# Kernel optimization log

Measured on AMD Instinct MI355X. Metric: run time of the kernel, lower is better.

Reference implementation:

```python
import jax, jax.numpy as jnp
import numpy as np

L = 16            # num_levels
F = 2             # features per level
T = 1 << 19       # hashmap size
BASE = 16         # base resolution
RES = 512         # desired_resolution (outer trilinear grid)
N_PTS = 262144

# 8 corner offsets of a unit cube, [8,3]
OFFS = np.array([[(c >> 0) & 1, (c >> 1) & 1, (c >> 2) & 1] for c in range(8)], dtype=np.uint32)
OFFS_J = jnp.asarray(OFFS)
OFFS_B = jnp.asarray(OFFS.astype(bool))
P1 = jnp.uint32(2654435761)
P2 = jnp.uint32(805459861)


def hash_encode(x01, table):
    """Instant-NGP multiresolution hash encoding. x01: [N,3] in [0,1]. table: [L,T,F]."""
    feats = []
    for l in range(L):
        res = BASE * (2 ** l)
        pos = x01 * res                      # [N,3]
        p0 = jnp.floor(pos)
        frac = pos - p0                      # [N,3]
        corners = p0.astype(jnp.uint32)[:, None, :] + OFFS_J[None]   # [N,8,3]
        if (res + 1) ** 3 <= T:              # dense level
            c = jnp.minimum(corners, jnp.uint32(res))
            idx = c[..., 0] + c[..., 1] * jnp.uint32(res + 1) + c[..., 2] * jnp.uint32((res + 1) * (res + 1))
        else:                                # hashed level (spatial hash, xor of primes)
            idx = corners[..., 0] ^ (corners[..., 1] * P1) ^ (corners[..., 2] * P2)
            idx = idx & jnp.uint32(T - 1)
        g = table[l][idx.astype(jnp.int32)]  # [N,8,F]
        w = jnp.where(OFFS_B[None], frac[:, None, :], 1.0 - frac[:, None, :]).prod(-1)  # [N,8]
        feats.append(jnp.einsum('nc,ncf->nf', w, g))
    return jnp.concatenate(feats, axis=-1)   # [N, L*F]


def mlp(x, W0, W1, W2):
    h = jax.nn.relu(x @ W0)
    h = jax.nn.relu(h @ W1)
    return h @ W2


def setup_inputs() -> dict:
    key = jax.random.key(0)
    k1, k2, k3, k4, k5 = jax.random.split(key, 5)
    xyz = jax.random.uniform(k1, (N_PTS, 3), dtype=jnp.float32, minval=-1.0, maxval=1.0)
    table = jax.random.uniform(k2, (L, T, F), dtype=jnp.float32, minval=-1e-4, maxval=1e-4)
    W0 = jax.random.normal(k3, (L * F, 64), dtype=jnp.float32) * (1.0 / np.sqrt(L * F))
    W1 = jax.random.normal(k4, (64, 64), dtype=jnp.float32) * (1.0 / 8.0)
    W2 = jax.random.normal(k5, (64, 8), dtype=jnp.float32) * (1.0 / 8.0)
    return {"xyz": xyz, "table": table, "W0": W0, "W1": W1, "W2": W2, "bound": 1}


def reference(xyz, table, W0, W1, W2, bound):
    xn = (xyz + bound) / (2 * bound)          # [N,3] in [0,1]
    coords = xn * RES
    c0 = jnp.clip(jnp.floor(coords), 0.0, RES - 1.0)   # [N,3] floats holding ints
    frac = coords - c0                         # u,v,w per-axis [N,3]
    out = jnp.zeros((xyz.shape[0], 8), dtype=xyz.dtype)
    for b in range(8):
        bits = np.array([(b >> 0) & 1, (b >> 1) & 1, (b >> 2) & 1], dtype=np.float32)
        cc = (c0 + bits) / RES                 # corner point normalized to [0,1]
        f = mlp(hash_encode(cc, table), W0, W1, W2)   # [N,8]
        w = jnp.where(bits.astype(bool), frac, 1.0 - frac).prod(-1)  # [N]
        out = out + w[:, None] * f
    return out
```

## Files before the change

### kernel.cpp

```cpp
#include <hip/hip_runtime.h>


typedef __attribute__((ext_vector_type(8))) short short8_t;
typedef __attribute__((ext_vector_type(4))) float f32x4;

static constexpr unsigned kT    = 1u << 19;
static constexpr unsigned kMask = kT - 1u;
static constexpr unsigned cP1   = 2654435761u;
static constexpr unsigned cP2   = 805459861u;
static constexpr int      BLOCK = 256;
static constexpr int      WOFF  = 4096;
static constexpr int      TOFF  = 4096;
static constexpr size_t   WS_NEED = ((size_t)TOFF + (1u << 21)) * 4;

static __device__ __forceinline__ unsigned bf16_rn(float x) {
    unsigned u = __float_as_uint(x);
    return (u + 0x7fffu + ((u >> 16) & 1u)) >> 16;
}

static __device__ __forceinline__ float2 bf2dec(unsigned u) {
    return make_float2(__uint_as_float(u << 16),
                       __uint_as_float(u & 0xffff0000u));
}

static __device__ __forceinline__ f32x4 mfma16(short8_t a, short8_t b, f32x4 c) {
    return __builtin_amdgcn_mfma_f32_16x16x32_bf16(a, b, c, 0, 0, 0);
}

__global__ void prep_w(const float* __restrict__ W0, const float* __restrict__ W1,
                       const float* __restrict__ W2, uint4* __restrict__ ws)
{
    const int t = blockIdx.x, lane = threadIdx.x;
    const int n = lane & 15, q = lane >> 4;
    unsigned hi[4];
    #pragma unroll
    for (int d = 0; d < 4; ++d) {
        unsigned h2[2];
        #pragma unroll
        for (int s = 0; s < 2; ++s) {
            const int j = d * 2 + s;
            float v;
            if (t < 4) {
                v = W0[(q * 8 + j) * 64 + t * 16 + n];
            } else {
                const int kp = (j < 4) ? (q * 4 + j) : (16 + q * 4 + (j - 4));
                if (t < 12) v = W1[(((t - 4) & 1) * 32 + kp) * 64 + ((t - 4) >> 1) * 16 + n];
                else        v = (n < 8) ? W2[((t - 12) * 32 + kp) * 8 + n] : 0.0f;
            }
            h2[s] = bf16_rn(v);
        }
        hi[d] = h2[0] | (h2[1] << 16);
    }
    ws[t * 64 + lane] = make_uint4(hi[0], hi[1], hi[2], hi[3]);
}

__global__ void conv_c(const float4* __restrict__ src, uint2* __restrict__ dst)
{
    const int i = blockIdx.x * 256 + threadIdx.x;
    const float4 v = src[i];
    dst[i] = make_uint2(bf16_rn(v.x) | (bf16_rn(v.y) << 16),
                        bf16_rn(v.z) | (bf16_rn(v.w) << 16));
}

__global__ void conv_f(const float2* __restrict__ src, unsigned* __restrict__ dst)
{
    const int i = blockIdx.x * 256 + threadIdx.x;
    const unsigned v = (1u << 20) - 1u - (unsigned)i;
    const int s = __clz((int)v) - 12;
    const unsigned fo = (1u << 20) - ((1u << 20) >> s);
    const unsigned j = (unsigned)i - fo;
    const float2 e = src[((size_t)(5 + s) << 19) + ((size_t)j << s)];
    dst[i] = bf16_rn(e.x) | (bf16_rn(e.y) << 16);
}

template<bool BT>
__global__ __launch_bounds__(BLOCK, 5)
void ngp_mfma(const float*  __restrict__ xyz,
              const float2* __restrict__ tbl,
              const int*    __restrict__ boundp,
              const unsigned* __restrict__ wsw,
              float*        __restrict__ out,
              int npts)
{
    __shared__ __align__(16) unsigned lds[7680];
    const int tid  = threadIdx.x;
    const int lane = tid & 63;
    const int wv   = tid >> 6;

    {
        const uint4* __restrict__ wsrc = (const uint4*)wsw;
        uint4* wdst = (uint4*)(lds + WOFF);
        #pragma unroll
        for (int k = 0; k < 4; ++k) {
            const int i = tid + k * 256;
            if (i < 896) wdst[i] = wsrc[i];
        }
    }

    const unsigned* __restrict__ tbx = wsw + TOFF;

    const int ge = blockIdx.x * BLOCK + tid;
    const int pt = ge >> 3;
    const int b  = ge & 7;

    const float bnd = (float)boundp[0];
    const float sc  = 0.5f / bnd;

    const float pxv = xyz[pt * 3 + 0];
    const float pyv = xyz[pt * 3 + 1];
    const float pzv = xyz[pt * 3 + 2];

    const float cxf = (pxv + bnd) * sc * 512.0f;
    const float cyf = (pyv + bnd) * sc * 512.0f;
    const float czf = (pzv + bnd) * sc * 512.0f;

    const float c0x = fminf(fmaxf(floorf(cxf), 0.0f), 511.0f);
    const float c0y = fminf(fmaxf(floorf(cyf), 0.0f), 511.0f);
    const float c0z = fminf(fmaxf(floorf(czf), 0.0f), 511.0f);
    const float frx = cxf - c0x;
    const float fry = cyf - c0y;
    const float frz = czf - c0z;

    const unsigned kx = (unsigned)c0x + (unsigned)(b & 1);
    const unsigned ky = (unsigned)c0y + (unsigned)((b >> 1) & 1);
    const unsigned kz = (unsigned)c0z + (unsigned)((b >> 2) & 1);

    const float wb = ((b & 1) ? frx : 1.0f - frx)
                   * ((b & 2) ? fry : 1.0f - fry)
                   * ((b & 4) ? frz : 1.0f - frz);

    const unsigned kyp = ky * cP1;
    const unsigned kzp = kz * cP2;
    const unsigned X   = kx ^ kyp ^ kzp;
    unsigned gfu[11];
    float2   gff[11];
    #pragma unroll
    for (int l = 5; l < 16; ++l) {
        const int s = l - 5;
        if (BT) {
            const unsigned base = (1u << 20) + ((1u << 20) - ((1u << 20) >> s));
            gfu[l - 5] = tbx[base + (X & (kMask >> s))];
        } else {
            const unsigned idx = ((kx << s) ^ (kyp << s) ^ (kzp << s)) & kMask;
            gff[l - 5] = tbl[(size_t)l * kT + idx];
        }
    }

    float2 gH[2][8];
    #pragma unroll
    for (int l = 3; l < 5; ++l) {
        const int d = 5 - l;
        const unsigned qx = kx >> d, qy = ky >> d, qz = kz >> d;
        const unsigned hy0 = qy * cP1, hy1 = hy0 + cP1;
        const unsigned hz0 = qz * cP2, hz1 = hz0 + cP2;
        const unsigned x1u = qx + 1u;
        unsigned hidx[8];
        hidx[0] = (qx  ^ hy0 ^ hz0) & kMask;  hidx[1] = (x1u ^ hy0 ^ hz0) & kMask;
        hidx[2] = (qx  ^ hy1 ^ hz0) & kMask;  hidx[3] = (x1u ^ hy1 ^ hz0) & kMask;
        hidx[4] = (qx  ^ hy0 ^ hz1) & kMask;  hidx[5] = (x1u ^ hy0 ^ hz1) & kMask;
        hidx[6] = (qx  ^ hy1 ^ hz1) & kMask;  hidx[7] = (x1u ^ hy1 ^ hz1) & kMask;
        if (BT) {
            const unsigned* __restrict__ base = tbx + (size_t)(l - 3) * kT;
            #pragma unroll
            for (int c = 0; c < 8; ++c) gH[l - 3][c] = bf2dec(base[hidx[c]]);
        } else {
            const float2* __restrict__ base = tbl + (size_t)l * kT;
            #pragma unroll
            for (int c = 0; c < 8; ++c) gH[l - 3][c] = base[hidx[c]];
        }
    }

    float2 gc[5];
    #pragma unroll
    for (int l = 0; l < 5; ++l) {
        const int d = 5 - l;
        const unsigned m = (1u << d) - 1u;
        const float inv = 1.0f / (float)(1 << d);
        const unsigned qx = kx >> d, qy = ky >> d, qz = kz >> d;
        const float fx = (float)(kx & m) * inv;
        const float fy = (float)(ky & m) * inv;
        const float fz = (float)(kz & m) * inv;
        float2 g0, g1, g2, g3, g4, g5, g6, g7;
        if (l < 3) {
            const unsigned res = 16u << l;
            const unsigned R = res + 1u, R2 = R * R;
            const unsigned x0 = (qx < res ? qx : res);
            const unsigned x1 = (qx + 1u < res ? qx + 1u : res);
            const unsigned y0 = (qy < res ? qy : res) * R;
            const unsigned y1 = (qy + 1u < res ? qy + 1u : res) * R;
            const unsigned z0 = (qz < res ? qz : res) * R2;
            const unsigned z1 = (qz + 1u < res ? qz + 1u : res) * R2;
            const float2* __restrict__ base = tbl + (size_t)l * kT;
            g0 = base[x0 + y0 + z0]; g1 = base[x1 + y0 + z0];
            g2 = base[x0 + y1 + z0]; g3 = base[x1 + y1 + z0];
            g4 = base[x0 + y0 + z1]; g5 = base[x1 + y0 + z1];
            g6 = base[x0 + y1 + z1]; g7 = base[x1 + y1 + z1];
        } else {
            g0 = gH[l - 3][0]; g1 = gH[l - 3][1]; g2 = gH[l - 3][2]; g3 = gH[l - 3][3];
            g4 = gH[l - 3][4]; g5 = gH[l - 3][5]; g6 = gH[l - 3][6]; g7 = gH[l - 3][7];
        }
        const float wx1 = fx, wx0 = 1.0f - fx;
        const float wy1 = fy, wy0 = 1.0f - fy;
        const float wz1 = fz, wz0 = 1.0f - fz;
        const float w00 = wx0 * wy0, w10 = wx1 * wy0, w01 = wx0 * wy1, w11 = wx1 * wy1;
        const float a0 = w00 * wz0, a1 = w10 * wz0, a2 = w01 * wz0, a3 = w11 * wz0;
        const float a4 = w00 * wz1, a5 = w10 * wz1, a6 = w01 * wz1, a7 = w11 * wz1;
        float vx = a0 * g0.x + a1 * g1.x + a2 * g2.x + a3 * g3.x
                 + a4 * g4.x + a5 * g5.x + a6 * g6.x + a7 * g7.x;
        float vy = a0 * g0.y + a1 * g1.y + a2 * g2.y + a3 * g3.y
                 + a4 * g4.y + a5 * g5.y + a6 * g6.y + a7 * g7.y;
        gc[l] = make_float2(vx, vy);
    }

    unsigned xd[16];
    #pragma unroll
    for (int l = 0; l < 5; ++l)
        xd[l] = bf16_rn(gc[l].x) | (bf16_rn(gc[l].y) << 16);
    #pragma unroll
    for (int l = 5; l < 16; ++l) {
        if (BT) xd[l] = gfu[l - 5];
        else    xd[l] = bf16_rn(gff[l - 5].x) | (bf16_rn(gff[l - 5].y) << 16);
    }
    uint4* xr = (uint4*)(lds + tid * 16);
    xr[0] = make_uint4(xd[0],  xd[1],  xd[2],  xd[3]);
    xr[1] = make_uint4(xd[4],  xd[5],  xd[6],  xd[7]);
    xr[2] = make_uint4(xd[8],  xd[9],  xd[10], xd[11]);
    xr[3] = make_uint4(xd[12], xd[13], xd[14], xd[15]);

    __syncthreads();

    const short8_t* __restrict__ wl = (const short8_t*)(lds + WOFF);
    const int col = lane & 15;
    const int q   = lane >> 4;
    const f32x4 zero = {0.0f, 0.0f, 0.0f, 0.0f};

    #pragma unroll 1
    for (int g = 0; g < 4; ++g) {
        const int ev = wv * 64 + g * 16 + col;
        const short8_t xb = *(const short8_t*)(lds + ev * 16 + q * 4);
        const float wbv = __shfl(wb, g * 16 + col, 64);

        unsigned hp0[4], hp1[4];
        #pragma unroll
        for (int mt = 0; mt < 4; ++mt) {
            f32x4 a = mfma16(wl[mt * 64 + lane], xb, zero);
            hp0[mt] = bf16_rn(fmaxf(a[0], 0.0f)) | (bf16_rn(fmaxf(a[1], 0.0f)) << 16);
            hp1[mt] = bf16_rn(fmaxf(a[2], 0.0f)) | (bf16_rn(fmaxf(a[3], 0.0f)) << 16);
        }
        uint4 u0 = make_uint4(hp0[0], hp1[0], hp0[1], hp1[1]);
        uint4 u1 = make_uint4(hp0[2], hp1[2], hp0[3], hp1[3]);
        short8_t bk0 = *(short8_t*)&u0;
        short8_t bk1 = *(short8_t*)&u1;

        #pragma unroll
        for (int mt = 0; mt < 4; ++mt) {
            f32x4 a = mfma16(wl[(4 + mt * 2) * 64 + lane], bk0, zero);
            a = mfma16(wl[(5 + mt * 2) * 64 + lane], bk1, a);
            hp0[mt] = bf16_rn(fmaxf(a[0], 0.0f)) | (bf16_rn(fmaxf(a[1], 0.0f)) << 16);
            hp1[mt] = bf16_rn(fmaxf(a[2], 0.0f)) | (bf16_rn(fmaxf(a[3], 0.0f)) << 16);
        }
        u0 = make_uint4(hp0[0], hp1[0], hp0[1], hp1[1]);
        u1 = make_uint4(hp0[2], hp1[2], hp0[3], hp1[3]);
        bk0 = *(short8_t*)&u0;
        bk1 = *(short8_t*)&u1;

        f32x4 a3 = mfma16(wl[12 * 64 + lane], bk0, zero);
        a3 = mfma16(wl[13 * 64 + lane], bk1, a3);

        float v0 = wbv * a3[0], v1 = wbv * a3[1], v2 = wbv * a3[2], v3 = wbv * a3[3];
        #pragma unroll
        for (int s = 1; s < 8; s <<= 1) {
            v0 += __shfl_xor(v0, s);
            v1 += __shfl_xor(v1, s);
            v2 += __shfl_xor(v2, s);
            v3 += __shfl_xor(v3, s);
        }
        if (((lane & 7) == 0) && q < 2) {
            const int p = (blockIdx.x * BLOCK + ev) >> 3;
            *(float4*)(out + p * 8 + q * 4) = make_float4(v0, v1, v2, v3);
        }
    }
}

extern "C" void kernel_launch(void* const* d_in, const int* in_sizes, int n_in,
                              void* d_out, int out_size, void* d_ws, size_t ws_size,
                              hipStream_t stream) {
    const float*  xyz = (const float*)d_in[0];
    const float2* tbl = (const float2*)d_in[1];
    const float*  W0  = (const float*)d_in[2];
    const float*  W1  = (const float*)d_in[3];
    const float*  W2  = (const float*)d_in[4];
    const int*    bnd = (const int*)d_in[5];
    float* out = (float*)d_out;

    const int npts  = in_sizes[0] / 3;
    const int total = npts * 8;
    const int grid  = total / BLOCK;

    hipLaunchKernelGGL(prep_w, dim3(14), dim3(64), 0, stream,
                       W0, W1, W2, (uint4*)d_ws);

    if (ws_size >= WS_NEED) {
        unsigned* tbx = (unsigned*)d_ws + TOFF;
        hipLaunchKernelGGL(conv_c, dim3((1 << 19) / 256), dim3(256), 0, stream,
                           (const float4*)(tbl + (size_t)3 * kT), (uint2*)tbx);
        hipLaunchKernelGGL(conv_f, dim3(((1 << 20) - (1 << 9)) / 256), dim3(256),
                           0, stream, tbl, tbx + (1 << 20));
        hipLaunchKernelGGL(ngp_mfma<true>, dim3(grid), dim3(BLOCK), 0, stream,
                           xyz, tbl, bnd, (const unsigned*)d_ws, out, npts);
    } else {
        hipLaunchKernelGGL(ngp_mfma<false>, dim3(grid), dim3(BLOCK), 0, stream,
                           xyz, tbl, bnd, (const unsigned*)d_ws, out, npts);
    }
}
```

Before: 233.1 us.

## Fuse prep kernels, keep MLP weights in registers, loop tiles per block

Merges the three preprocessing launches (weight packing and two bf16 table conversions) into one kernel to cut launch overhead. The main kernel now holds the 14 weight fragments in VGPRs instead of LDS, processes four 256-element tiles per block, XOR-swizzles the LDS feature rows to reduce bank conflicts, and uses the hardware v_cvt_pk_bf16_f32 instruction for packing. __syncthreads is replaced by a waitcnt, which relies on each wave reading only its own rows. Launch bounds drop to 4 waves per SIMD to make room for the extra registers.

```diff
diff --git a/kernel.cpp b/kernel.cpp
--- a/kernel.cpp
+++ b/kernel.cpp
@@ -9,7 +9,7 @@
 static constexpr unsigned cP1   = 2654435761u;
 static constexpr unsigned cP2   = 805459861u;
 static constexpr int      BLOCK = 256;
-static constexpr int      WOFF  = 4096;
+static constexpr int      ITER  = 4;
 static constexpr int      TOFF  = 4096;
 static constexpr size_t   WS_NEED = ((size_t)TOFF + (1u << 21)) * 4;
 
@@ -23,261 +23,269 @@
                        __uint_as_float(u & 0xffff0000u));
 }
 
+static __device__ __forceinline__ unsigned cvtpk(float lo, float hi) {
+    unsigned r;
+    asm("v_cvt_pk_bf16_f32 %0, %1, %2" : "=v"(r) : "v"(lo), "v"(hi));
+    return r;
+}
+
 static __device__ __forceinline__ f32x4 mfma16(short8_t a, short8_t b, f32x4 c) {
     return __builtin_amdgcn_mfma_f32_16x16x32_bf16(a, b, c, 0, 0, 0);
 }
 
-__global__ void prep_w(const float* __restrict__ W0, const float* __restrict__ W1,
-                       const float* __restrict__ W2, uint4* __restrict__ ws)
+__global__ __launch_bounds__(256)
+void prep_all(const float* __restrict__ W0, const float* __restrict__ W1,
+              const float* __restrict__ W2, const float2* __restrict__ tbl,
+              unsigned* __restrict__ ws, int ncc, int ncf)
 {
-    const int t = blockIdx.x, lane = threadIdx.x;
-    const int n = lane & 15, q = lane >> 4;
-    unsigned hi[4];
-    #pragma unroll
-    for (int d = 0; d < 4; ++d) {
-        unsigned h2[2];
-        #pragma unroll
-        for (int s = 0; s < 2; ++s) {
-            const int j = d * 2 + s;
-            float v;
-            if (t < 4) {
-                v = W0[(q * 8 + j) * 64 + t * 16 + n];
-            } else {
-                const int kp = (j < 4) ? (q * 4 + j) : (16 + q * 4 + (j - 4));
-                if (t < 12) v = W1[(((t - 4) & 1) * 32 + kp) * 64 + ((t - 4) >> 1) * 16 + n];
-                else        v = (n < 8) ? W2[((t - 12) * 32 + kp) * 8 + n] : 0.0f;
-            }
-            h2[s] = bf16_rn(v);
-        }
-        hi[d] = h2[0] | (h2[1] << 16);
+    const int bx = blockIdx.x, tid = threadIdx.x;
+    if (bx < ncc) {
+        const int i = bx * 256 + tid;
+        const float4 v = ((const float4*)(tbl + (size_t)3 * kT))[i];
+        ((uint2*)(ws + TOFF))[i] =
+            make_uint2(bf16_rn(v.x) | (bf16_rn(v.y) << 16),
+                       bf16_rn(v.z) | (bf16_rn(v.w) << 16));
+    } else if (bx < ncc + ncf) {
+        const int i = (bx - ncc) * 256 + tid;
+        const unsigned vv = (1u << 20) - 1u - (unsigned)i;
+        const int s = __clz((int)vv) - 12;
+        const unsigned fo = (1u << 20) - ((1u << 20) >> s);
+        const unsigned j = (unsigned)i - fo;
+        const float2 e = tbl[((size_t)(5 + s) << 19) + ((size_t)j << s)];
+        (ws + TOFF + (1u << 20))[i] = bf16_rn(e.x) | (bf16_rn(e.y) << 16);
+    } else {
+        const int t = (bx - ncc - ncf) * 4 + (tid >> 6);
+        if (t >= 14) return;
+        const int lane = tid & 63;
+        const int n = lane & 15, q = lane >> 4;
+        unsigned hi[4];
+        #pragma unroll
+        for (int d = 0; d < 4; ++d) {
+            unsigned h2[2];
+            #pragma unroll
+            for (int s = 0; s < 2; ++s) {
+                const int j = d * 2 + s;
+                float v;
+                if (t < 4) {
+                    v = W0[(q * 8 + j) * 64 + t * 16 + n];
+                } else {
+                    const int kp = (j < 4) ? (q * 4 + j) : (16 + q * 4 + (j - 4));
+                    if (t < 12) v = W1[(((t - 4) & 1) * 32 + kp) * 64 + ((t - 4) >> 1) * 16 + n];
+                    else        v = (n < 8) ? W2[((t - 12) * 32 + kp) * 8 + n] : 0.0f;
+                }
+                h2[s] = bf16_rn(v);
+            }
+            hi[d] = h2[0] | (h2[1] << 16);
+        }
+        ((uint4*)ws)[t * 64 + lane] = make_uint4(hi[0], hi[1], hi[2], hi[3]);
     }
-    ws[t * 64 + lane] = make_uint4(hi[0], hi[1], hi[2], hi[3]);
-}
-
-__global__ void conv_c(const float4* __restrict__ src, uint2* __restrict__ dst)
-{
-    const int i = blockIdx.x * 256 + threadIdx.x;
-    const float4 v = src[i];
-    dst[i] = make_uint2(bf16_rn(v.x) | (bf16_rn(v.y) << 16),
-                        bf16_rn(v.z) | (bf16_rn(v.w) << 16));
-}
-
-__global__ void conv_f(const float2* __restrict__ src, unsigned* __restrict__ dst)
-{
-    const int i = blockIdx.x * 256 + threadIdx.x;
-    const unsigned v = (1u << 20) - 1u - (unsigned)i;
-    const int s = __clz((int)v) - 12;
-    const unsigned fo = (1u << 20) - ((1u << 20) >> s);
-    const unsigned j = (unsigned)i - fo;
-    const float2 e = src[((size_t)(5 + s) << 19) + ((size_t)j << s)];
-    dst[i] = bf16_rn(e.x) | (bf16_rn(e.y) << 16);
 }
 
 template<bool BT>
-__global__ __launch_bounds__(BLOCK, 5)
+__global__ __launch_bounds__(BLOCK, 4)
 void ngp_mfma(const float*  __restrict__ xyz,
               const float2* __restrict__ tbl,
               const int*    __restrict__ boundp,
               const unsigned* __restrict__ wsw,
               float*        __restrict__ out,
-              int npts)
+              int ntiles)
 {
-    __shared__ __align__(16) unsigned lds[7680];
+    __shared__ __align__(16) unsigned lds[4096];
     const int tid  = threadIdx.x;
     const int lane = tid & 63;
     const int wv   = tid >> 6;
-
+    const int col  = lane & 15;
+    const int q    = lane >> 4;
+
+    short8_t w[14];
     {
-        const uint4* __restrict__ wsrc = (const uint4*)wsw;
-        uint4* wdst = (uint4*)(lds + WOFF);
-        #pragma unroll
-        for (int k = 0; k < 4; ++k) {
-            const int i = tid + k * 256;
-            if (i < 896) wdst[i] = wsrc[i];
-        }
+        const short8_t* __restrict__ wfr = (const short8_t*)wsw;
+        #pragma unroll
+        for (int t = 0; t < 14; ++t) w[t] = wfr[t * 64 + lane];
     }
 
     const unsigned* __restrict__ tbx = wsw + TOFF;
-
-    const int ge = blockIdx.x * BLOCK + tid;
-    const int pt = ge >> 3;
-    const int b  = ge & 7;
-
     const float bnd = (float)boundp[0];
     const float sc  = 0.5f / bnd;
-
-    const float pxv = xyz[pt * 3 + 0];
-    const float pyv = xyz[pt * 3 + 1];
-    const float pzv = xyz[pt * 3 + 2];
-
-    const float cxf = (pxv + bnd) * sc * 512.0f;
-    const float cyf = (pyv + bnd) * sc * 512.0f;
-    const float czf = (pzv + bnd) * sc * 512.0f;
-
-    const float c0x = fminf(fmaxf(floorf(cxf), 0.0f), 511.0f);
-    const float c0y = fminf(fmaxf(floorf(cyf), 0.0f), 511.0f);
-    const float c0z = fminf(fmaxf(floorf(czf), 0.0f), 511.0f);
-    const float frx = cxf - c0x;
-    const float fry = cyf - c0y;
-    const float frz = czf - c0z;
-
-    const unsigned kx = (unsigned)c0x + (unsigned)(b & 1);
-    const unsigned ky = (unsigned)c0y + (unsigned)((b >> 1) & 1);
-    const unsigned kz = (unsigned)c0z + (unsigned)((b >> 2) & 1);
-
-    const float wb = ((b & 1) ? frx : 1.0f - frx)
-                   * ((b & 2) ? fry : 1.0f - fry)
-                   * ((b & 4) ? frz : 1.0f - frz);
-
-    const unsigned kyp = ky * cP1;
-    const unsigned kzp = kz * cP2;
-    const unsigned X   = kx ^ kyp ^ kzp;
-    unsigned gfu[11];
-    float2   gff[11];
-    #pragma unroll
-    for (int l = 5; l < 16; ++l) {
-        const int s = l - 5;
-        if (BT) {
-            const unsigned base = (1u << 20) + ((1u << 20) - ((1u << 20) >> s));
-            gfu[l - 5] = tbx[base + (X & (kMask >> s))];
-        } else {
-            const unsigned idx = ((kx << s) ^ (kyp << s) ^ (kzp << s)) & kMask;
-            gff[l - 5] = tbl[(size_t)l * kT + idx];
-        }
-    }
-
-    float2 gH[2][8];
-    #pragma unroll
-    for (int l = 3; l < 5; ++l) {
-        const int d = 5 - l;
-        const unsigned qx = kx >> d, qy = ky >> d, qz = kz >> d;
-        const unsigned hy0 = qy * cP1, hy1 = hy0 + cP1;
-        const unsigned hz0 = qz * cP2, hz1 = hz0 + cP2;
-        const unsigned x1u = qx + 1u;
-        unsigned hidx[8];
-        hidx[0] = (qx  ^ hy0 ^ hz0) & kMask;  hidx[1] = (x1u ^ hy0 ^ hz0) & kMask;
-        hidx[2] = (qx  ^ hy1 ^ hz0) & kMask;  hidx[3] = (x1u ^ hy1 ^ hz0) & kMask;
-        hidx[4] = (qx  ^ hy0 ^ hz1) & kMask;  hidx[5] = (x1u ^ hy0 ^ hz1) & kMask;
-        hidx[6] = (qx  ^ hy1 ^ hz1) & kMask;  hidx[7] = (x1u ^ hy1 ^ hz1) & kMask;
-        if (BT) {
-            const unsigned* __restrict__ base = tbx + (size_t)(l - 3) * kT;
+    const f32x4 zero = {0.0f, 0.0f, 0.0f, 0.0f};
+    const int swz = (tid ^ (tid >> 2) ^ (tid >> 4)) & 3;
+
+    #pragma unroll 1
+    for (int it = 0; it < ITER; ++it) {
+        const int tile = blockIdx.x * ITER + it;
+        if (tile >= ntiles) break;
+
+        const int ge = tile * BLOCK + tid;
+        const int pt = ge >> 3;
+        const int b  = ge & 7;
+
+        const float cxf = (xyz[pt * 3 + 0] + bnd) * sc * 512.0f;
+        const float cyf = (xyz[pt * 3 + 1] + bnd) * sc * 512.0f;
+        const float czf = (xyz[pt * 3 + 2] + bnd) * sc * 512.0f;
+
+        const float c0x = fminf(fmaxf(floorf(cxf), 0.0f), 511.0f);
+        const float c0y = fminf(fmaxf(floorf(cyf), 0.0f), 511.0f);
+        const float c0z = fminf(fmaxf(floorf(czf), 0.0f), 511.0f);
+        const float frx = cxf - c0x;
+        const float fry = cyf - c0y;
+        const float frz = czf - c0z;
+
+        const unsigned kx = (unsigned)c0x + (unsigned)(b & 1);
+        const unsigned ky = (unsigned)c0y + (unsigned)((b >> 1) & 1);
+        const unsigned kz = (unsigned)c0z + (unsigned)((b >> 2) & 1);
+
+        const float wb = ((b & 1) ? frx : 1.0f - frx)
+                       * ((b & 2) ? fry : 1.0f - fry)
+                       * ((b & 4) ? frz : 1.0f - frz);
+
+        const unsigned kyp = ky * cP1;
+        const unsigned kzp = kz * cP2;
+        const unsigned X   = kx ^ kyp ^ kzp;
+        unsigned gfu[11];
+        float2   gff[11];
+        #pragma unroll
+        for (int l = 5; l < 16; ++l) {
+            const int s = l - 5;
+            if (BT) {
+                const unsigned base = (1u << 20) + ((1u << 20) - ((1u << 20) >> s));
+                gfu[l - 5] = tbx[base + (X & (kMask >> s))];
+            } else {
+                const unsigned idx = ((kx << s) ^ (kyp << s) ^ (kzp << s)) & kMask;
+                gff[l - 5] = tbl[(size_t)l * kT + idx];
+            }
+        }
+
+        float2 gH[2][8];
+        #pragma unroll
+        for (int l = 3; l < 5; ++l) {
+            const int d = 5 - l;
+            const unsigned qx = kx >> d, qy = ky >> d, qz = kz >> d;
+            const unsigned hy0 = qy * cP1, hy1 = hy0 + cP1;
+            const unsigned hz0 = qz * cP2, hz1 = hz0 + cP2;
+            const unsigned x1u = qx + 1u;
+            unsigned hidx[8];
+            hidx[0] = (qx  ^ hy0 ^ hz0) & kMask;  hidx[1] = (x1u ^ hy0 ^ hz0) & kMask;
+            hidx[2] = (qx  ^ hy1 ^ hz0) & kMask;  hidx[3] = (x1u ^ hy1 ^ hz0) & kMask;
+            hidx[4] = (qx  ^ hy0 ^ hz1) & kMask;  hidx[5] = (x1u ^ hy0 ^ hz1) & kMask;
+            hidx[6] = (qx  ^ hy1 ^ hz1) & kMask;  hidx[7] = (x1u ^ hy1 ^ hz1) & kMask;
+            if (BT) {
+                const unsigned* __restrict__ base = tbx + (size_t)(l - 3) * kT;
+                #pragma unroll
+                for (int c = 0; c < 8; ++c) gH[l - 3][c] = bf2dec(base[hidx[c]]);
+            } else {
+                const float2* __restrict__ base = tbl + (size_t)l * kT;
+                #pragma unroll
+                for (int c = 0; c < 8; ++c) gH[l - 3][c] = base[hidx[c]];
+            }
+        }
+
+        float2 gc[5];
+        #pragma unroll
+        for (int l = 0; l < 5; ++l) {
+            const int d = 5 - l;
+            const unsigned m = (1u << d) - 1u;
+            const float inv = 1.0f / (float)(1 << d);
+            const unsigned qx = kx >> d, qy = ky >> d, qz = kz >> d;
+            const float fx = (float)(kx & m) * inv;
+            const float fy = (float)(ky & m) * inv;
+            const float fz = (float)(kz & m) * inv;
+            float2 g0, g1, g2, g3, g4, g5, g6, g7;
+            if (l < 3) {
+                const unsigned res = 16u << l;
+                const unsigned R = res + 1u, R2 = R * R;
+                const unsigned x0 = (qx < res ? qx : res);
+                const unsigned x1 = (qx + 1u < res ? qx + 1u : res);
+                const unsigned y0 = (qy < res ? qy : res) * R;
+                const unsigned y1 = (qy + 1u < res ? qy + 1u : res) * R;
+                const unsigned z0 = (qz < res ? qz : res) * R2;
+                const unsigned z1 = (qz + 1u < res ? qz + 1u : res) * R2;
+                const float2* __restrict__ base = tbl + (size_t)l * kT;
+                g0 = base[x0 + y0 + z0]; g1 = base[x1 + y0 + z0];
+                g2 = base[x0 + y1 + z0]; g3 = base[x1 + y1 + z0];
+                g4 = base[x0 + y0 + z1]; g5 = base[x1 + y0 + z1];
+                g6 = base[x0 + y1 + z1]; g7 = base[x1 + y1 + z1];
+            } else {
+                g0 = gH[l - 3][0]; g1 = gH[l - 3][1]; g2 = gH[l - 3][2]; g3 = gH[l - 3][3];
+                g4 = gH[l - 3][4]; g5 = gH[l - 3][5]; g6 = gH[l - 3][6]; g7 = gH[l - 3][7];
+            }
+            const float wx1 = fx, wx0 = 1.0f - fx;
+            const float wy1 = fy, wy0 = 1.0f - fy;
+            const float wz1 = fz, wz0 = 1.0f - fz;
+            const float w00 = wx0 * wy0, w10 = wx1 * wy0, w01 = wx0 * wy1, w11 = wx1 * wy1;
+            const float a0 = w00 * wz0, a1 = w10 * wz0, a2 = w01 * wz0, a3 = w11 * wz0;
+            const float a4 = w00 * wz1, a5 = w10 * wz1, a6 = w01 * wz1, a7 = w11 * wz1;
+            float vx = a0 * g0.x + a1 * g1.x + a2 * g2.x + a3 * g3.x
+                     + a4 * g4.x + a5 * g5.x + a6 * g6.x + a7 * g7.x;
+            float vy = a0 * g0.y + a1 * g1.y + a2 * g2.y + a3 * g3.y
+                     + a4 * g4.y + a5 * g5.y + a6 * g6.y + a7 * g7.y;
+            gc[l] = make_float2(vx, vy);
+        }
+
+        unsigned xd[16];
+        #pragma unroll
+        for (int l = 0; l < 5; ++l)
+            xd[l] = cvtpk(gc[l].x, gc[l].y);
+        #pragma unroll
+        for (int l = 5; l < 16; ++l) {
+            if (BT) xd[l] = gfu[l - 5];
+            else    xd[l] = cvtpk(gff[l - 5].x, gff[l - 5].y);
+        }
+        {
+            uint4* xrow = (uint4*)(lds + tid * 16);
+            xrow[swz]     = make_uint4(xd[0],  xd[1],  xd[2],  xd[3]);
+            xrow[swz ^ 1] = make_uint4(xd[4],  xd[5],  xd[6],  xd[7]);
+            xrow[swz ^ 2] = make_uint4(xd[8],  xd[9],  xd[10], xd[11]);
+            xrow[swz ^ 3] = make_uint4(xd[12], xd[13], xd[14], xd[15]);
+        }
+
+        asm volatile("s_waitcnt lgkmcnt(0)" ::: "memory");
+
+        #pragma unroll 1
+        for (int g = 0; g < 4; ++g) {
+            const int ev  = wv * 64 + g * 16 + col;
+            const int esw = ((ev ^ (ev >> 2) ^ (ev >> 4)) & 3) ^ q;
+            const short8_t xb = *(const short8_t*)(lds + ev * 16 + esw * 4);
+            const float wbv = __shfl(wb, g * 16 + col, 64);
+
+            unsigned hp0[4], hp1[4];
             #pragma unroll
-            for (int c = 0; c < 8; ++c) gH[l - 3][c] = bf2dec(base[hidx[c]]);
-        } else {
-            const float2* __restrict__ base = tbl + (size_t)l * kT;
+            for (int mt = 0; mt < 4; ++mt) {
+                f32x4 a = mfma16(w[mt], xb, zero);
+                hp0[mt] = cvtpk(fmaxf(a[0], 0.0f), fmaxf(a[1], 0.0f));
+                hp1[mt] = cvtpk(fmaxf(a[2], 0.0f), fmaxf(a[3], 0.0f));
+            }
+            uint4 u0 = make_uint4(hp0[0], hp1[0], hp0[1], hp1[1]);
+            uint4 u1 = make_uint4(hp0[2], hp1[2], hp0[3], hp1[3]);
+            short8_t bk0 = *(short8_t*)&u0;
+            short8_t bk1 = *(short8_t*)&u1;
+
             #pragma unroll
-            for (int c = 0; c < 8; ++c) gH[l - 3][c] = base[hidx[c]];
-        }
-    }
-
-    float2 gc[5];
-    #pragma unroll
-    for (int l = 0; l < 5; ++l) {
-        const int d = 5 - l;
-        const unsigned m = (1u << d) - 1u;
-        const float inv = 1.0f / (float)(1 << d);
-        const unsigned qx = kx >> d, qy = ky >> d, qz = kz >> d;
-        const float fx = (float)(kx & m) * inv;
-        const float fy = (float)(ky & m) * inv;
-        const float fz = (float)(kz & m) * inv;
-        float2 g0, g1, g2, g3, g4, g5, g6, g7;
-        if (l < 3) {
-            const unsigned res = 16u << l;
-            const unsigned R = res + 1u, R2 = R * R;
-            const unsigned x0 = (qx < res ? qx : res);
-            const unsigned x1 = (qx + 1u < res ? qx + 1u : res);
-            const unsigned y0 = (qy < res ? qy : res) * R;
-            const unsigned y1 = (qy + 1u < res ? qy + 1u : res) * R;
-            const unsigned z0 = (qz < res ? qz : res) * R2;
-            const unsigned z1 = (qz + 1u < res ? qz + 1u : res) * R2;
-            const float2* __restrict__ base = tbl + (size_t)l * kT;
-            g0 = base[x0 + y0 + z0]; g1 = base[x1 + y0 + z0];
-            g2 = base[x0 + y1 + z0]; g3 = base[x1 + y1 + z0];
-            g4 = base[x0 + y0 + z1]; g5 = base[x1 + y0 + z1];
-            g6 = base[x0 + y1 + z1]; g7 = base[x1 + y1 + z1];
-        } else {
-            g0 = gH[l - 3][0]; g1 = gH[l - 3][1]; g2 = gH[l - 3][2]; g3 = gH[l - 3][3];
-            g4 = gH[l - 3][4]; g5 = gH[l - 3][5]; g6 = gH[l - 3][6]; g7 = gH[l - 3][7];
-        }
-        const float wx1 = fx, wx0 = 1.0f - fx;
-        const float wy1 = fy, wy0 = 1.0f - fy;
-        const float wz1 = fz, wz0 = 1.0f - fz;
-        const float w00 = wx0 * wy0, w10 = wx1 * wy0, w01 = wx0 * wy1, w11 = wx1 * wy1;
-        const float a0 = w00 * wz0, a1 = w10 * wz0, a2 = w01 * wz0, a3 = w11 * wz0;
-        const float a4 = w00 * wz1, a5 = w10 * wz1, a6 = w01 * wz1, a7 = w11 * wz1;
-        float vx = a0 * g0.x + a1 * g1.x + a2 * g2.x + a3 * g3.x
-                 + a4 * g4.x + a5 * g5.x + a6 * g6.x + a7 * g7.x;
-        float vy = a0 * g0.y + a1 * g1.y + a2 * g2.y + a3 * g3.y
-                 + a4 * g4.y + a5 * g5.y + a6 * g6.y + a7 * g7.y;
-        gc[l] = make_float2(vx, vy);
-    }
-
-    unsigned xd[16];
-    #pragma unroll
-    for (int l = 0; l < 5; ++l)
-        xd[l] = bf16_rn(gc[l].x) | (bf16_rn(gc[l].y) << 16);
-    #pragma unroll
-    for (int l = 5; l < 16; ++l) {
-        if (BT) xd[l] = gfu[l - 5];
-        else    xd[l] = bf16_rn(gff[l - 5].x) | (bf16_rn(gff[l - 5].y) << 16);
-    }
-    uint4* xr = (uint4*)(lds + tid * 16);
-    xr[0] = make_uint4(xd[0],  xd[1],  xd[2],  xd[3]);
-    xr[1] = make_uint4(xd[4],  xd[5],  xd[6],  xd[7]);
-    xr[2] = make_uint4(xd[8],  xd[9],  xd[10], xd[11]);
-    xr[3] = make_uint4(xd[12], xd[13], xd[14], xd[15]);
-
-    __syncthreads();
-
-    const short8_t* __restrict__ wl = (const short8_t*)(lds + WOFF);
-    const int col = lane & 15;
-    const int q   = lane >> 4;
-    const f32x4 zero = {0.0f, 0.0f, 0.0f, 0.0f};
-
-    #pragma unroll 1
-    for (int g = 0; g < 4; ++g) {
-        const int ev = wv * 64 + g * 16 + col;
-        const short8_t xb = *(const short8_t*)(lds + ev * 16 + q * 4);
-        const float wbv = __shfl(wb, g * 16 + col, 64);
-
-        unsigned hp0[4], hp1[4];
-        #pragma unroll
-        for (int mt = 0; mt < 4; ++mt) {
-            f32x4 a = mfma16(wl[mt * 64 + lane], xb, zero);
-            hp0[mt] = bf16_rn(fmaxf(a[0], 0.0f)) | (bf16_rn(fmaxf(a[1], 0.0f)) << 16);
-            hp1[mt] = bf16_rn(fmaxf(a[2], 0.0f)) | (bf16_rn(fmaxf(a[3], 0.0f)) << 16);
-        }
-        uint4 u0 = make_uint4(hp0[0], hp1[0], hp0[1], hp1[1]);
-        uint4 u1 = make_uint4(hp0[2], hp1[2], hp0[3], hp1[3]);
-        short8_t bk0 = *(short8_t*)&u0;
-        short8_t bk1 = *(short8_t*)&u1;
-
-        #pragma unroll
-        for (int mt = 0; mt < 4; ++mt) {
-            f32x4 a = mfma16(wl[(4 + mt * 2) * 64 + lane], bk0, zero);
-            a = mfma16(wl[(5 + mt * 2) * 64 + lane], bk1, a);
-            hp0[mt] = bf16_rn(fmaxf(a[0], 0.0f)) | (bf16_rn(fmaxf(a[1], 0.0f)) << 16);
-            hp1[mt] = bf16_rn(fmaxf(a[2], 0.0f)) | (bf16_rn(fmaxf(a[3], 0.0f)) << 16);
-        }
-        u0 = make_uint4(hp0[0], hp1[0], hp0[1], hp1[1]);
-        u1 = make_uint4(hp0[2], hp1[2], hp0[3], hp1[3]);
-        bk0 = *(short8_t*)&u0;
-        bk1 = *(short8_t*)&u1;
-
-        f32x4 a3 = mfma16(wl[12 * 64 + lane], bk0, zero);
-        a3 = mfma16(wl[13 * 64 + lane], bk1, a3);
-
-        float v0 = wbv * a3[0], v1 = wbv * a3[1], v2 = wbv * a3[2], v3 = wbv * a3[3];
-        #pragma unroll
-        for (int s = 1; s < 8; s <<= 1) {
-            v0 += __shfl_xor(v0, s);
-            v1 += __shfl_xor(v1, s);
-            v2 += __shfl_xor(v2, s);
-            v3 += __shfl_xor(v3, s);
-        }
-        if (((lane & 7) == 0) && q < 2) {
-            const int p = (blockIdx.x * BLOCK + ev) >> 3;
-            *(float4*)(out + p * 8 + q * 4) = make_float4(v0, v1, v2, v3);
+            for (int mt = 0; mt < 4; ++mt) {
+                f32x4 a = mfma16(w[4 + mt * 2], bk0, zero);
+                a = mfma16(w[5 + mt * 2], bk1, a);
+                hp0[mt] = cvtpk(fmaxf(a[0], 0.0f), fmaxf(a[1], 0.0f));
+                hp1[mt] = cvtpk(fmaxf(a[2], 0.0f), fmaxf(a[3], 0.0f));
+            }
+            u0 = make_uint4(hp0[0], hp1[0], hp0[1], hp1[1]);
+            u1 = make_uint4(hp0[2], hp1[2], hp0[3], hp1[3]);
+            bk0 = *(short8_t*)&u0;
+            bk1 = *(short8_t*)&u1;
+
+            f32x4 a3 = mfma16(w[12], bk0, zero);
+            a3 = mfma16(w[13], bk1, a3);
+
+            float v0 = wbv * a3[0], v1 = wbv * a3[1], v2 = wbv * a3[2], v3 = wbv * a3[3];
+            #pragma unroll
+            for (int s = 1; s < 8; s <<= 1) {
+                v0 += __shfl_xor(v0, s);
+                v1 += __shfl_xor(v1, s);
+                v2 += __shfl_xor(v2, s);
+                v3 += __shfl_xor(v3, s);
+            }
+            if (((lane & 7) == 0) && q < 2) {
+                const int p = (tile * BLOCK + ev) >> 3;
+                *(float4*)(out + p * 8 + q * 4) = make_float4(v0, v1, v2, v3);
+            }
         }
     }
 }
@@ -293,23 +301,23 @@
     const int*    bnd = (const int*)d_in[5];
     float* out = (float*)d_out;
 
-    const int npts  = in_sizes[0] / 3;
-    const int total = npts * 8;
-    const int grid  = total / BLOCK;
-
-    hipLaunchKernelGGL(prep_w, dim3(14), dim3(64), 0, stream,
-                       W0, W1, W2, (uint4*)d_ws);
-
-    if (ws_size >= WS_NEED) {
-        unsigned* tbx = (unsigned*)d_ws + TOFF;
-        hipLaunchKernelGGL(conv_c, dim3((1 << 19) / 256), dim3(256), 0, stream,
-                           (const float4*)(tbl + (size_t)3 * kT), (uint2*)tbx);
-        hipLaunchKernelGGL(conv_f, dim3(((1 << 20) - (1 << 9)) / 256), dim3(256),
-                           0, stream, tbl, tbx + (1 << 20));
+    const int npts   = in_sizes[0] / 3;
+    const int total  = npts * 8;
+    const int ntiles = total / BLOCK;
+    const int grid   = (ntiles + ITER - 1) / ITER;
+
+    const bool big = (ws_size >= WS_NEED);
+    const int ncc = big ? (1 << 19) / 256 : 0;
+    const int ncf = big ? ((1 << 20) - (1 << 9)) / 256 : 0;
+
+    hipLaunchKernelGGL(prep_all, dim3(ncc + ncf + 4), dim3(256), 0, stream,
+                       W0, W1, W2, tbl, (unsigned*)d_ws, ncc, ncf);
+
+    if (big) {
         hipLaunchKernelGGL(ngp_mfma<true>, dim3(grid), dim3(BLOCK), 0, stream,
-                           xyz, tbl, bnd, (const unsigned*)d_ws, out, npts);
+                           xyz, tbl, bnd, (const unsigned*)d_ws, out, ntiles);
     } else {
         hipLaunchKernelGGL(ngp_mfma<false>, dim3(grid), dim3(BLOCK), 0, stream,
-                           xyz, tbl, bnd, (const unsigned*)d_ws, out, npts);
+                           xyz, tbl, bnd, (const unsigned*)d_ws, out, ntiles);
     }
 }
```

Result: slower. 259.8 us (+11.5%).
